# Performance work log

Hardware: AMD Instinct MI355X
Metric: run time of the kernel (lower is better)

Reference implementation:

```python
import jax, jax.numpy as jnp
import numpy as np

B, T, C, H = 2, 2048, 1024, 16
HD = C // H  # head dim 64


def setup_inputs() -> dict:
    key = jax.random.key(0)
    k1, k2, k3, k4, k5 = jax.random.split(key, 5)
    s = 0.02
    return {
        "x": jax.random.normal(k1, (B, T, C), dtype=jnp.float32),
        "w_attn": jax.random.normal(k2, (3 * C, C), dtype=jnp.float32) * s,
        "b_attn": jax.random.normal(k3, (3 * C,), dtype=jnp.float32) * s,
        "w_proj": jax.random.normal(k4, (C, C), dtype=jnp.float32) * s,
        "b_proj": jax.random.normal(k5, (C,), dtype=jnp.float32) * s,
    }


def reference(x, w_attn, b_attn, w_proj, b_proj):
    b, t, c = x.shape
    h, hd = H, c // H
    # qkv projection: [B,T,3C]
    qkv = x @ w_attn.T + b_attn
    q, k, v = jnp.split(qkv, 3, axis=-1)
    # [B,H,T,HD]
    q = q.reshape(b, t, h, hd).transpose(0, 2, 1, 3)
    k = k.reshape(b, t, h, hd).transpose(0, 2, 1, 3)
    v = v.reshape(b, t, h, hd).transpose(0, 2, 1, 3)
    scale = 1.0 / jnp.sqrt(jnp.asarray(hd, dtype=x.dtype))
    att = jnp.einsum("bhqd,bhkd->bhqk", q, k) * scale  # [B,H,T,T]
    causal = jnp.tril(jnp.ones((t, t), dtype=bool))
    att = jnp.where(causal, att, jnp.asarray(-jnp.inf, dtype=att.dtype))
    att = jax.nn.softmax(att, axis=-1)
    # dropout p=0.0 (eval): no-op
    y = jnp.einsum("bhqk,bhkd->bhqd", att, v)  # [B,H,T,HD]
    y = y.transpose(0, 2, 1, 3).reshape(b, t, c)
    return y @ w_proj.T + b_proj
```

## Files before the change

kernel.cpp:

```cpp
#include <hip/hip_runtime.h>
#include <hip/hip_bf16.h>

typedef __attribute__((ext_vector_type(4))) float f32x4;
typedef __attribute__((ext_vector_type(8))) short bh8;

#define DEVI static __device__ __forceinline__

constexpr int Bn = 2, T = 2048, C = 1024, H = 16, HD = 64;
constexpr int BH = Bn * H;
constexpr int M  = Bn * T;
constexpr float QSC = 0.125f * 1.44269504088896f;

DEVI unsigned short f2bf(float f) {
  unsigned int u = __builtin_bit_cast(unsigned int, f);
  u += 0x7FFFu + ((u >> 16) & 1u);
  return (unsigned short)(u >> 16);
}

DEVI unsigned int cvtpk(float lo, float hi) {
  unsigned int r;
  asm("v_cvt_pk_bf16_f32 %0, %1, %2" : "=v"(r) : "v"(lo), "v"(hi));
  return r;
}

DEVI float fexp2(float x) {
  float r;
  asm("v_exp_f32 %0, %1" : "=v"(r) : "v"(x));
  return r;
}

DEVI void gload16(const void* g, void* l) {
  __builtin_amdgcn_global_load_lds((const __attribute__((address_space(1))) void*)g,
                                   (__attribute__((address_space(3))) void*)l,
                                   16, 0, 0);
}

__global__ __launch_bounds__(256) void cvt_all(const float* __restrict__ x,
                                               const float* __restrict__ wa,
                                               const float* __restrict__ wp,
                                               unsigned short* __restrict__ out) {
  constexpr size_t n0 = (size_t)M * C;
  constexpr size_t n1 = n0 + (size_t)3 * C * C;
  const size_t i = ((size_t)blockIdx.x * 256 + threadIdx.x) * 4;
  const float* src;
  size_t off;
  if (i < n0)      { src = x;  off = i; }
  else if (i < n1) { src = wa; off = i - n0; }
  else             { src = wp; off = i - n1; }
  const float4 v = *(const float4*)(src + off);
  ushort4 o;
  o.x = f2bf(v.x); o.y = f2bf(v.y); o.z = f2bf(v.z); o.w = f2bf(v.w);
  *(ushort4*)(out + i) = o;
}

template <int EPI>
__global__ __launch_bounds__(512, 6) void gemm_bt(
    const unsigned short* __restrict__ A, const unsigned short* __restrict__ Bw,
    const float* __restrict__ bias, int N, int K,
    unsigned short* __restrict__ Qb, unsigned short* __restrict__ Kb,
    unsigned short* __restrict__ Vb, float* __restrict__ Outf) {
  __shared__ unsigned short As[128 * 64];
  __shared__ unsigned short Bs[128 * 64];

  const int tid  = threadIdx.x;
  const int lane = tid & 63;
  const int wid  = tid >> 6;
  const int wm = wid >> 1, wn = wid & 1;
  const int m0 = blockIdx.y * 128;
  const int n0 = blockIdx.x * 128;
  const int l15 = lane & 15, l4 = lane >> 4;

  const int srow = lane >> 3;
  const int gp   = lane & 7;

  const unsigned short* Ab = A + (size_t)m0 * K;
  const unsigned short* Bb = Bw + (size_t)n0 * K;

  f32x4 acc[2][4] = {};

  for (int kt = 0; kt < K; kt += 64) {
    __syncthreads();
#pragma unroll
    for (int sl = 0; sl < 2; ++sl) {
      const int row = wid * 16 + sl * 8 + srow;
      const int gs  = gp ^ (row & 7);
      gload16(Ab + (size_t)row * K + kt + gs * 8, &As[(wid * 16 + sl * 8) * 64]);
      gload16(Bb + (size_t)row * K + kt + gs * 8, &Bs[(wid * 16 + sl * 8) * 64]);
    }
    __syncthreads();

#pragma unroll
    for (int kk = 0; kk < 2; ++kk) {
      bh8 af[2], bfr[4];
#pragma unroll
      for (int i = 0; i < 2; ++i) {
        const int row  = wm * 32 + i * 16 + l15;
        const int gran = kk * 4 + l4;
        af[i] = *(const bh8*)&As[row * 64 + ((gran ^ (row & 7)) * 8)];
      }
#pragma unroll
      for (int j = 0; j < 4; ++j) {
        const int row  = wn * 64 + j * 16 + l15;
        const int gran = kk * 4 + l4;
        bfr[j] = *(const bh8*)&Bs[row * 64 + ((gran ^ (row & 7)) * 8)];
      }
#pragma unroll
      for (int i = 0; i < 2; ++i)
#pragma unroll
        for (int j = 0; j < 4; ++j)
          acc[i][j] = __builtin_amdgcn_mfma_f32_16x16x32_bf16(af[i], bfr[j],
                                                              acc[i][j], 0, 0, 0);
    }
  }

  const int rbase = m0 + wm * 32 + (l4 << 2);
  const int cbase = n0 + wn * 64 + l15;

  if (EPI == 0) {
#pragma unroll
    for (int j = 0; j < 4; ++j) {
      const int n = cbase + j * 16;
      const float bv = bias[n];
#pragma unroll
      for (int i = 0; i < 2; ++i)
#pragma unroll
        for (int r = 0; r < 4; ++r) {
          const int m = rbase + i * 16 + r;
          Outf[(size_t)m * N + n] = acc[i][j][r] + bv;
        }
    }
  } else {
#pragma unroll
    for (int j = 0; j < 4; ++j) {
      const int n = cbase + j * 16;
      const float bv = bias[n];
      const int part = n >> 10;
      const int nn = n & 1023;
      const int h = nn >> 6, d = nn & 63;
#pragma unroll
      for (int i = 0; i < 2; ++i)
#pragma unroll
        for (int r = 0; r < 4; ++r) {
          const int m = rbase + i * 16 + r;
          const int b = m >> 11, t = m & (T - 1);
          const int bh = b * H + h;
          const float val = acc[i][j][r] + bv;
          if (part == 0)
            Qb[((size_t)(bh * T + t)) * HD + d] = f2bf(val * QSC);
          else if (part == 1)
            Kb[((size_t)(bh * T + t)) * HD + d] = f2bf(val);
          else {
            const int kp  = t & 127;
            const int kap = (kp & ~31) | (((kp >> 2) & 3) << 3) |
                            (((kp >> 4) & 1) << 2) | (kp & 3);
            const int tp  = (t & ~127) | kap;
            Vb[((size_t)(bh * HD + d)) * T + tp] = f2bf(val);
          }
        }
    }
  }
}

__global__ __launch_bounds__(512, 2) void attn(
    const unsigned short* __restrict__ Qb, const unsigned short* __restrict__ Kb,
    const unsigned short* __restrict__ Vb, unsigned short* __restrict__ Yb) {
  __shared__ unsigned short Ks[2][2][64 * 64];
  __shared__ unsigned short Vs[2][2][64 * 64];
  __shared__ float Mg[4][64][37];

  const int tid  = threadIdx.x;
  const int lane = tid & 63;
  const int wid  = tid >> 6;
  const int g    = wid >> 2;
  const int wv   = wid & 3;
  const int bh   = blockIdx.x;
  const int b = bh >> 4, h = bh & 15;
  const int qa = blockIdx.y;
  const int p0n = qa + 1;

  const int l4  = lane >> 4;
  const int l15 = lane & 15;

  const unsigned short* Kbh = Kb + (size_t)bh * T * HD;
  const unsigned short* Vbh = Vb + (size_t)bh * HD * T;

  const int sr = lane >> 3, sg = lane & 7;

  bh8 qk[2][2];
  auto loadQ = [&](int tile) {
#pragma unroll
    for (int c = 0; c < 2; ++c) {
      const size_t qo =
          ((size_t)(bh * T + tile * 128 + wv * 32 + c * 16 + l15)) * HD + l4 * 8;
      qk[c][0] = *(const bh8*)&Qb[qo];
      qk[c][1] = *(const bh8*)&Qb[qo + 32];
    }
  };
  loadQ(qa);

  f32x4 o[2][4] = {};
  float mcur[2] = {-1e30f, -1e30f}, lsum[2] = {0.f, 0.f};

  auto stage = [&](int buf, int kt) {
#pragma unroll
    for (int sl = 0; sl < 2; ++sl) {
      const int row = wv * 16 + sl * 8 + sr;
      const int gs  = sg ^ (row & 7);
      gload16(Kbh + (size_t)(kt + row) * HD + gs * 8,
              &Ks[g][buf][(wv * 16 + sl * 8) * 64]);
      gload16(Vbh + (size_t)row * T + kt + gs * 8,
              &Vs[g][buf][(wv * 16 + sl * 8) * 64]);
    }
  };

  auto flush = [&](int qt) {
    __syncthreads();
    if (g == 1) {
#pragma unroll
      for (int c = 0; c < 2; ++c)
#pragma unroll
        for (int dj = 0; dj < 4; ++dj)
#pragma unroll
          for (int r = 0; r < 4; ++r)
            Mg[wv][lane][c * 16 + dj * 4 + r] = o[c][dj][r];
      Mg[wv][lane][32] = mcur[0]; Mg[wv][lane][33] = mcur[1];
      Mg[wv][lane][34] = lsum[0]; Mg[wv][lane][35] = lsum[1];
    }
    __syncthreads();
    if (g == 0) {
#pragma unroll
      for (int c = 0; c < 2; ++c) {
        const float mb = Mg[wv][lane][32 + c];
        const float lb = Mg[wv][lane][34 + c];
        const float m  = fmaxf(mcur[c], mb);
        const float wa = fexp2(mcur[c] - m);
        const float wb = fexp2(mb - m);
        const float inv = 1.f / (lsum[c] * wa + lb * wb);
        const int t = qt * 128 + wv * 32 + c * 16 + l15;
#pragma unroll
        for (int dj = 0; dj < 4; ++dj) {
          const float* mo = &Mg[wv][lane][c * 16 + dj * 4];
          ushort4 hw;
          hw.x = f2bf((o[c][dj][0] * wa + mo[0] * wb) * inv);
          hw.y = f2bf((o[c][dj][1] * wa + mo[1] * wb) * inv);
          hw.z = f2bf((o[c][dj][2] * wa + mo[2] * wb) * inv);
          hw.w = f2bf((o[c][dj][3] * wa + mo[3] * wb) * inv);
          *(ushort4*)&Yb[((size_t)(b * T + t)) * C + h * HD + dj * 16 + l4 * 4] = hw;
        }
      }
    }
    __syncthreads();
  };

  stage(0, g * 64);
  __syncthreads();

  int cur = 0;
  for (int i = 0; i < 17; ++i) {
    if (i == p0n) {
      flush(qa);
      mcur[0] = mcur[1] = -1e30f; lsum[0] = lsum[1] = 0.f;
#pragma unroll
      for (int c = 0; c < 2; ++c)
#pragma unroll
        for (int dj = 0; dj < 4; ++dj) o[c][dj] = f32x4{0.f, 0.f, 0.f, 0.f};
      loadQ(15 - qa);
    }

    if (i < 16) {
      const int ni  = i + 1;
      const int nli = (ni >= p0n) ? ni - p0n : ni;
      stage(cur ^ 1, (2 * nli + g) * 64);
    }

    const int li = (i >= p0n) ? i - p0n : i;
    const int qt = (i >= p0n) ? 15 - qa : qa;
    const int kt = (2 * li + g) * 64;

    f32x4 s[2][4] = {};
#pragma unroll
    for (int kk = 0; kk < 2; ++kk) {
      __builtin_amdgcn_s_setprio(1);
#pragma unroll
      for (int j = 0; j < 4; ++j) {
        const int row  = j * 16 + l15;
        const int gran = kk * 4 + l4;
        const bh8 kfr = *(const bh8*)&Ks[g][cur][row * 64 + ((gran ^ (row & 7)) * 8)];
        s[0][j] = __builtin_amdgcn_mfma_f32_16x16x32_bf16(kfr, qk[0][kk], s[0][j], 0, 0, 0);
        s[1][j] = __builtin_amdgcn_mfma_f32_16x16x32_bf16(kfr, qk[1][kk], s[1][j], 0, 0, 0);
      }
      __builtin_amdgcn_s_setprio(0);
    }

    if (kt >= qt * 128) {
      const int kbase = kt - qt * 128;
#pragma unroll
      for (int c = 0; c < 2; ++c) {
        const int qloc = wv * 32 + c * 16 + l15;
#pragma unroll
        for (int j = 0; j < 4; ++j)
#pragma unroll
          for (int r = 0; r < 4; ++r) {
            const int kvl = kbase + j * 16 + l4 * 4 + r;
            if (kvl > qloc) s[c][j][r] = -1e30f;
          }
      }
    }

    float mx[2];
#pragma unroll
    for (int c = 0; c < 2; ++c) {
      float m = fmaxf(fmaxf(s[c][0][0], s[c][0][1]), fmaxf(s[c][0][2], s[c][0][3]));
#pragma unroll
      for (int j = 1; j < 4; ++j)
        m = fmaxf(m, fmaxf(fmaxf(s[c][j][0], s[c][j][1]), fmaxf(s[c][j][2], s[c][j][3])));
      m = fmaxf(m, __shfl_xor(m, 16));
      m = fmaxf(m, __shfl_xor(m, 32));
      mx[c] = m;
    }
    const bool grow = (mx[0] > mcur[0] + 8.f) || (mx[1] > mcur[1] + 8.f);
    if (__any(grow)) {
#pragma unroll
      for (int c = 0; c < 2; ++c) {
        const float mnew  = fmaxf(mcur[c], mx[c]);
        const float alpha = fexp2(mcur[c] - mnew);
        mcur[c] = mnew; lsum[c] *= alpha;
#pragma unroll
        for (int dj = 0; dj < 4; ++dj) o[c][dj] *= alpha;
      }
    }
#pragma unroll
    for (int c = 0; c < 2; ++c) {
      float ps = 0.f;
#pragma unroll
      for (int j = 0; j < 4; ++j)
#pragma unroll
        for (int r = 0; r < 4; ++r) {
          const float p = fexp2(s[c][j][r] - mcur[c]);
          s[c][j][r] = p;
          ps += p;
        }
      ps += __shfl_xor(ps, 16);
      ps += __shfl_xor(ps, 32);
      lsum[c] += ps;
    }

#pragma unroll
    for (int kk2 = 0; kk2 < 2; ++kk2) {
      const int gran = kk2 * 4 + l4;
      int4 pw0, pw1;
      pw0.x = cvtpk(s[0][2 * kk2][0], s[0][2 * kk2][1]);
      pw0.y = cvtpk(s[0][2 * kk2][2], s[0][2 * kk2][3]);
      pw0.z = cvtpk(s[0][2 * kk2 + 1][0], s[0][2 * kk2 + 1][1]);
      pw0.w = cvtpk(s[0][2 * kk2 + 1][2], s[0][2 * kk2 + 1][3]);
      pw1.x = cvtpk(s[1][2 * kk2][0], s[1][2 * kk2][1]);
      pw1.y = cvtpk(s[1][2 * kk2][2], s[1][2 * kk2][3]);
      pw1.z = cvtpk(s[1][2 * kk2 + 1][0], s[1][2 * kk2 + 1][1]);
      pw1.w = cvtpk(s[1][2 * kk2 + 1][2], s[1][2 * kk2 + 1][3]);
      const bh8 pf0 = __builtin_bit_cast(bh8, pw0);
      const bh8 pf1 = __builtin_bit_cast(bh8, pw1);
      __builtin_amdgcn_s_setprio(1);
#pragma unroll
      for (int dj = 0; dj < 4; ++dj) {
        const int row = dj * 16 + l15;
        const bh8 vf = *(const bh8*)&Vs[g][cur][row * 64 + ((gran ^ (row & 7)) * 8)];
        o[0][dj] = __builtin_amdgcn_mfma_f32_16x16x32_bf16(vf, pf0, o[0][dj], 0, 0, 0);
        o[1][dj] = __builtin_amdgcn_mfma_f32_16x16x32_bf16(vf, pf1, o[1][dj], 0, 0, 0);
      }
      __builtin_amdgcn_s_setprio(0);
    }

    __syncthreads();
    cur ^= 1;
  }

  flush(15 - qa);
}

extern "C" void kernel_launch(void* const* d_in, const int* in_sizes, int n_in,
                              void* d_out, int out_size, void* d_ws, size_t ws_size,
                              hipStream_t stream) {
  const float* x      = (const float*)d_in[0];
  const float* w_attn = (const float*)d_in[1];
  const float* b_attn = (const float*)d_in[2];
  const float* w_proj = (const float*)d_in[3];
  const float* b_proj = (const float*)d_in[4];
  float* out = (float*)d_out;

  unsigned short* xb  = (unsigned short*)d_ws;
  unsigned short* wab = xb  + (size_t)M * C;
  unsigned short* wpb = wab + (size_t)3 * C * C;
  unsigned short* Qb  = wpb + (size_t)C * C;
  unsigned short* Kb  = Qb  + (size_t)M * C;
  unsigned short* Vb  = Kb  + (size_t)M * C;
  unsigned short* Yb  = xb;

  constexpr int CVT_BLOCKS = (M * C + 3 * C * C + C * C) / 1024;
  cvt_all<<<dim3(CVT_BLOCKS), 256, 0, stream>>>(x, w_attn, w_proj, xb);

  gemm_bt<1><<<dim3(3 * C / 128, M / 128), 512, 0, stream>>>(
      xb, wab, b_attn, 3 * C, C, Qb, Kb, Vb, nullptr);

  attn<<<dim3(BH, 8), 512, 0, stream>>>(Qb, Kb, Vb, Yb);

  gemm_bt<0><<<dim3(C / 128, M / 128), 512, 0, stream>>>(
      Yb, wpb, b_proj, C, C, nullptr, nullptr, nullptr, out);
}
```

Measured before the change: 105.5 us.

## Split attention work across 16 waves with one 16-row Q chunk each

The attention kernel now launches 1024 threads per block (16 waves) instead of 512, and each wave handles 16 query rows instead of 32. Per-wave register state (scores, outputs, max and sum) is halved, K/V staging is spread over twice as many waves, and the merge buffer shrinks to match. The goal is more waves in flight and lower register pressure to hide latency. In exchange, each K/V fragment read from LDS is reused across fewer MFMAs, and block-wide barriers now have to synchronise more waves.

```diff
diff --git a/kernel.cpp b/kernel.cpp
--- a/kernel.cpp
+++ b/kernel.cpp
@@ -161,18 +161,18 @@
   }
 }
 
-__global__ __launch_bounds__(512, 2) void attn(
+__global__ __launch_bounds__(1024, 4) void attn(
     const unsigned short* __restrict__ Qb, const unsigned short* __restrict__ Kb,
     const unsigned short* __restrict__ Vb, unsigned short* __restrict__ Yb) {
   __shared__ unsigned short Ks[2][2][64 * 64];
   __shared__ unsigned short Vs[2][2][64 * 64];
-  __shared__ float Mg[4][64][37];
+  __shared__ float Mg[8][64][19];
 
   const int tid  = threadIdx.x;
   const int lane = tid & 63;
   const int wid  = tid >> 6;
-  const int g    = wid >> 2;
-  const int wv   = wid & 3;
+  const int g    = wid >> 3;
+  const int wv   = wid & 7;
   const int bh   = blockIdx.x;
   const int b = bh >> 4, h = bh & 15;
   const int qa = blockIdx.y;
@@ -186,67 +186,54 @@
 
   const int sr = lane >> 3, sg = lane & 7;
 
-  bh8 qk[2][2];
+  bh8 qk[2];
   auto loadQ = [&](int tile) {
-#pragma unroll
-    for (int c = 0; c < 2; ++c) {
-      const size_t qo =
-          ((size_t)(bh * T + tile * 128 + wv * 32 + c * 16 + l15)) * HD + l4 * 8;
-      qk[c][0] = *(const bh8*)&Qb[qo];
-      qk[c][1] = *(const bh8*)&Qb[qo + 32];
-    }
+    const size_t qo =
+        ((size_t)(bh * T + tile * 128 + wv * 16 + l15)) * HD + l4 * 8;
+    qk[0] = *(const bh8*)&Qb[qo];
+    qk[1] = *(const bh8*)&Qb[qo + 32];
   };
   loadQ(qa);
 
-  f32x4 o[2][4] = {};
-  float mcur[2] = {-1e30f, -1e30f}, lsum[2] = {0.f, 0.f};
+  f32x4 o[4] = {};
+  float mcur = -1e30f, lsum = 0.f;
 
   auto stage = [&](int buf, int kt) {
-#pragma unroll
-    for (int sl = 0; sl < 2; ++sl) {
-      const int row = wv * 16 + sl * 8 + sr;
-      const int gs  = sg ^ (row & 7);
-      gload16(Kbh + (size_t)(kt + row) * HD + gs * 8,
-              &Ks[g][buf][(wv * 16 + sl * 8) * 64]);
-      gload16(Vbh + (size_t)row * T + kt + gs * 8,
-              &Vs[g][buf][(wv * 16 + sl * 8) * 64]);
-    }
+    const int row = wv * 8 + sr;
+    const int gs  = sg ^ (row & 7);
+    gload16(Kbh + (size_t)(kt + row) * HD + gs * 8, &Ks[g][buf][(wv * 8) * 64]);
+    gload16(Vbh + (size_t)row * T + kt + gs * 8,    &Vs[g][buf][(wv * 8) * 64]);
   };
 
   auto flush = [&](int qt) {
     __syncthreads();
     if (g == 1) {
 #pragma unroll
-      for (int c = 0; c < 2; ++c)
-#pragma unroll
-        for (int dj = 0; dj < 4; ++dj)
-#pragma unroll
-          for (int r = 0; r < 4; ++r)
-            Mg[wv][lane][c * 16 + dj * 4 + r] = o[c][dj][r];
-      Mg[wv][lane][32] = mcur[0]; Mg[wv][lane][33] = mcur[1];
-      Mg[wv][lane][34] = lsum[0]; Mg[wv][lane][35] = lsum[1];
+      for (int dj = 0; dj < 4; ++dj)
+#pragma unroll
+        for (int r = 0; r < 4; ++r)
+          Mg[wv][lane][dj * 4 + r] = o[dj][r];
+      Mg[wv][lane][16] = mcur;
+      Mg[wv][lane][17] = lsum;
     }
     __syncthreads();
     if (g == 0) {
-#pragma unroll
-      for (int c = 0; c < 2; ++c) {
-        const float mb = Mg[wv][lane][32 + c];
-        const float lb = Mg[wv][lane][34 + c];
-        const float m  = fmaxf(mcur[c], mb);
-        const float wa = fexp2(mcur[c] - m);
-        const float wb = fexp2(mb - m);
-        const float inv = 1.f / (lsum[c] * wa + lb * wb);
-        const int t = qt * 128 + wv * 32 + c * 16 + l15;
-#pragma unroll
-        for (int dj = 0; dj < 4; ++dj) {
-          const float* mo = &Mg[wv][lane][c * 16 + dj * 4];
-          ushort4 hw;
-          hw.x = f2bf((o[c][dj][0] * wa + mo[0] * wb) * inv);
-          hw.y = f2bf((o[c][dj][1] * wa + mo[1] * wb) * inv);
-          hw.z = f2bf((o[c][dj][2] * wa + mo[2] * wb) * inv);
-          hw.w = f2bf((o[c][dj][3] * wa + mo[3] * wb) * inv);
-          *(ushort4*)&Yb[((size_t)(b * T + t)) * C + h * HD + dj * 16 + l4 * 4] = hw;
-        }
+      const float mb = Mg[wv][lane][16];
+      const float lb = Mg[wv][lane][17];
+      const float m  = fmaxf(mcur, mb);
+      const float wa = fexp2(mcur - m);
+      const float wb = fexp2(mb - m);
+      const float inv = 1.f / (lsum * wa + lb * wb);
+      const int t = qt * 128 + wv * 16 + l15;
+#pragma unroll
+      for (int dj = 0; dj < 4; ++dj) {
+        const float* mo = &Mg[wv][lane][dj * 4];
+        ushort4 hw;
+        hw.x = f2bf((o[dj][0] * wa + mo[0] * wb) * inv);
+        hw.y = f2bf((o[dj][1] * wa + mo[1] * wb) * inv);
+        hw.z = f2bf((o[dj][2] * wa + mo[2] * wb) * inv);
+        hw.w = f2bf((o[dj][3] * wa + mo[3] * wb) * inv);
+        *(ushort4*)&Yb[((size_t)(b * T + t)) * C + h * HD + dj * 16 + l4 * 4] = hw;
       }
     }
     __syncthreads();
@@ -259,11 +246,9 @@
   for (int i = 0; i < 17; ++i) {
     if (i == p0n) {
       flush(qa);
-      mcur[0] = mcur[1] = -1e30f; lsum[0] = lsum[1] = 0.f;
-#pragma unroll
-      for (int c = 0; c < 2; ++c)
-#pragma unroll
-        for (int dj = 0; dj < 4; ++dj) o[c][dj] = f32x4{0.f, 0.f, 0.f, 0.f};
+      mcur = -1e30f; lsum = 0.f;
+#pragma unroll
+      for (int dj = 0; dj < 4; ++dj) o[dj] = f32x4{0.f, 0.f, 0.f, 0.f};
       loadQ(15 - qa);
     }
 
@@ -277,7 +262,7 @@
     const int qt = (i >= p0n) ? 15 - qa : qa;
     const int kt = (2 * li + g) * 64;
 
-    f32x4 s[2][4] = {};
+    f32x4 s[4] = {};
 #pragma unroll
     for (int kk = 0; kk < 2; ++kk) {
       __builtin_amdgcn_s_setprio(1);
@@ -286,86 +271,64 @@
         const int row  = j * 16 + l15;
         const int gran = kk * 4 + l4;
         const bh8 kfr = *(const bh8*)&Ks[g][cur][row * 64 + ((gran ^ (row & 7)) * 8)];
-        s[0][j] = __builtin_amdgcn_mfma_f32_16x16x32_bf16(kfr, qk[0][kk], s[0][j], 0, 0, 0);
-        s[1][j] = __builtin_amdgcn_mfma_f32_16x16x32_bf16(kfr, qk[1][kk], s[1][j], 0, 0, 0);
+        s[j] = __builtin_amdgcn_mfma_f32_16x16x32_bf16(kfr, qk[kk], s[j], 0, 0, 0);
       }
       __builtin_amdgcn_s_setprio(0);
     }
 
     if (kt >= qt * 128) {
       const int kbase = kt - qt * 128;
-#pragma unroll
-      for (int c = 0; c < 2; ++c) {
-        const int qloc = wv * 32 + c * 16 + l15;
-#pragma unroll
-        for (int j = 0; j < 4; ++j)
-#pragma unroll
-          for (int r = 0; r < 4; ++r) {
-            const int kvl = kbase + j * 16 + l4 * 4 + r;
-            if (kvl > qloc) s[c][j][r] = -1e30f;
-          }
-      }
-    }
-
-    float mx[2];
-#pragma unroll
-    for (int c = 0; c < 2; ++c) {
-      float m = fmaxf(fmaxf(s[c][0][0], s[c][0][1]), fmaxf(s[c][0][2], s[c][0][3]));
-#pragma unroll
-      for (int j = 1; j < 4; ++j)
-        m = fmaxf(m, fmaxf(fmaxf(s[c][j][0], s[c][j][1]), fmaxf(s[c][j][2], s[c][j][3])));
-      m = fmaxf(m, __shfl_xor(m, 16));
-      m = fmaxf(m, __shfl_xor(m, 32));
-      mx[c] = m;
-    }
-    const bool grow = (mx[0] > mcur[0] + 8.f) || (mx[1] > mcur[1] + 8.f);
-    if (__any(grow)) {
-#pragma unroll
-      for (int c = 0; c < 2; ++c) {
-        const float mnew  = fmaxf(mcur[c], mx[c]);
-        const float alpha = fexp2(mcur[c] - mnew);
-        mcur[c] = mnew; lsum[c] *= alpha;
-#pragma unroll
-        for (int dj = 0; dj < 4; ++dj) o[c][dj] *= alpha;
-      }
-    }
-#pragma unroll
-    for (int c = 0; c < 2; ++c) {
-      float ps = 0.f;
+      const int qloc  = wv * 16 + l15;
 #pragma unroll
       for (int j = 0; j < 4; ++j)
 #pragma unroll
         for (int r = 0; r < 4; ++r) {
-          const float p = fexp2(s[c][j][r] - mcur[c]);
-          s[c][j][r] = p;
-          ps += p;
+          const int kvl = kbase + j * 16 + l4 * 4 + r;
+          if (kvl > qloc) s[j][r] = -1e30f;
         }
-      ps += __shfl_xor(ps, 16);
-      ps += __shfl_xor(ps, 32);
-      lsum[c] += ps;
-    }
+    }
+
+    float mx = fmaxf(fmaxf(s[0][0], s[0][1]), fmaxf(s[0][2], s[0][3]));
+#pragma unroll
+    for (int j = 1; j < 4; ++j)
+      mx = fmaxf(mx, fmaxf(fmaxf(s[j][0], s[j][1]), fmaxf(s[j][2], s[j][3])));
+    mx = fmaxf(mx, __shfl_xor(mx, 16));
+    mx = fmaxf(mx, __shfl_xor(mx, 32));
+    if (__any(mx > mcur + 8.f)) {
+      const float mnew  = fmaxf(mcur, mx);
+      const float alpha = fexp2(mcur - mnew);
+      mcur = mnew; lsum *= alpha;
+#pragma unroll
+      for (int dj = 0; dj < 4; ++dj) o[dj] *= alpha;
+    }
+    float ps = 0.f;
+#pragma unroll
+    for (int j = 0; j < 4; ++j)
+#pragma unroll
+      for (int r = 0; r < 4; ++r) {
+        const float p = fexp2(s[j][r] - mcur);
+        s[j][r] = p;
+        ps += p;
+      }
+    ps += __shfl_xor(ps, 16);
+    ps += __shfl_xor(ps, 32);
+    lsum += ps;
 
 #pragma unroll
     for (int kk2 = 0; kk2 < 2; ++kk2) {
       const int gran = kk2 * 4 + l4;
-      int4 pw0, pw1;
-      pw0.x = cvtpk(s[0][2 * kk2][0], s[0][2 * kk2][1]);
-      pw0.y = cvtpk(s[0][2 * kk2][2], s[0][2 * kk2][3]);
-      pw0.z = cvtpk(s[0][2 * kk2 + 1][0], s[0][2 * kk2 + 1][1]);
-      pw0.w = cvtpk(s[0][2 * kk2 + 1][2], s[0][2 * kk2 + 1][3]);
-      pw1.x = cvtpk(s[1][2 * kk2][0], s[1][2 * kk2][1]);
-      pw1.y = cvtpk(s[1][2 * kk2][2], s[1][2 * kk2][3]);
-      pw1.z = cvtpk(s[1][2 * kk2 + 1][0], s[1][2 * kk2 + 1][1]);
-      pw1.w = cvtpk(s[1][2 * kk2 + 1][2], s[1][2 * kk2 + 1][3]);
-      const bh8 pf0 = __builtin_bit_cast(bh8, pw0);
-      const bh8 pf1 = __builtin_bit_cast(bh8, pw1);
+      int4 pw;
+      pw.x = cvtpk(s[2 * kk2][0], s[2 * kk2][1]);
+      pw.y = cvtpk(s[2 * kk2][2], s[2 * kk2][3]);
+      pw.z = cvtpk(s[2 * kk2 + 1][0], s[2 * kk2 + 1][1]);
+      pw.w = cvtpk(s[2 * kk2 + 1][2], s[2 * kk2 + 1][3]);
+      const bh8 pf = __builtin_bit_cast(bh8, pw);
       __builtin_amdgcn_s_setprio(1);
 #pragma unroll
       for (int dj = 0; dj < 4; ++dj) {
         const int row = dj * 16 + l15;
         const bh8 vf = *(const bh8*)&Vs[g][cur][row * 64 + ((gran ^ (row & 7)) * 8)];
-        o[0][dj] = __builtin_amdgcn_mfma_f32_16x16x32_bf16(vf, pf0, o[0][dj], 0, 0, 0);
-        o[1][dj] = __builtin_amdgcn_mfma_f32_16x16x32_bf16(vf, pf1, o[1][dj], 0, 0, 0);
+        o[dj] = __builtin_amdgcn_mfma_f32_16x16x32_bf16(vf, pf, o[dj], 0, 0, 0);
       }
       __builtin_amdgcn_s_setprio(0);
     }
@@ -401,7 +364,7 @@
   gemm_bt<1><<<dim3(3 * C / 128, M / 128), 512, 0, stream>>>(
       xb, wab, b_attn, 3 * C, C, Qb, Kb, Vb, nullptr);
 
-  attn<<<dim3(BH, 8), 512, 0, stream>>>(Qb, Kb, Vb, Yb);
+  attn<<<dim3(BH, 8), 1024, 0, stream>>>(Qb, Kb, Vb, Yb);
 
   gemm_bt<0><<<dim3(C / 128, M / 128), 512, 0, stream>>>(
       Yb, wpb, b_proj, C, C, nullptr, nullptr, nullptr, out);
```

Result: faster. 102.8 us (-2.6%).
